# Kernel optimization log

Hardware: AMD Instinct MI355X
Metric: run time of the kernel (lower is better)

The kernel has to match this reference:

```python
import jax, jax.numpy as jnp
import numpy as np

B, T, D = 4, 2048, 2048
NUM_EXPERTS = 64
TOP_K = 2


def setup_inputs() -> dict:
    key = jax.random.key(0)
    k_x, k_n, k_wg, k_wn = jax.random.split(key, 4)
    x = jax.random.normal(k_x, (B, T, D), dtype=jnp.float32)
    noise_eps = jax.random.normal(k_n, (B, T, NUM_EXPERTS), dtype=jnp.float32)
    # nn.Linear(D, E, bias=False): weight [E, D]; store transposed [D, E] for einsum
    scale = 1.0 / np.sqrt(D)
    w_gate = jax.random.uniform(k_wg, (D, NUM_EXPERTS), jnp.float32, -scale, scale)
    w_noise = jax.random.uniform(k_wn, (D, NUM_EXPERTS), jnp.float32, -scale, scale)
    return {"x": x, "noise_eps": noise_eps, "w_gate": w_gate, "w_noise": w_noise}


def reference(x, noise_eps, w_gate, w_noise):
    # gate + noisy logits: softplus(w_noise(x)) * randn_like (noise_eps passed in)
    logits = jnp.einsum("btd,de->bte", x, w_gate)
    noise = jax.nn.softplus(jnp.einsum("btd,de->bte", x, w_noise)) * noise_eps
    logits = logits + noise

    # top-k over experts
    top_k_logits, top_k_indices = jax.lax.top_k(logits, TOP_K)  # [B,T,K]

    # scatter(-inf fill) + softmax == softmax over top-k values scattered into E slots
    one_hot = jax.nn.one_hot(top_k_indices, NUM_EXPERTS, dtype=logits.dtype)  # [B,T,K,E]
    router_probs = jnp.einsum("btk,btke->bte", jax.nn.softmax(top_k_logits, axis=-1), one_hot)

    # per-expert mask: [num_tokens, K, E] -> permute(1,0,2) -> [K, num_tokens, E]
    exp_mask = one_hot.reshape(B * T, TOP_K, NUM_EXPERTS).transpose(1, 0, 2).astype(jnp.int32)
    return router_probs, top_k_indices, exp_mask
```

## Files before the change

kernel.cpp:

```cpp
#include <hip/hip_runtime.h>
#include <math.h>

#define DD     2048
#define EE     64
#define NTOK   8192
#define BM     64
#define KSPLIT 4
#define KQ     512
#define BK     64
#define NCH    (KQ / BK)

#define PROB_OFF 0
#define IDX_OFF  524288
#define MASK_OFF 540672
#define MASK_K_STRIDE (NTOK * EE)

#define XBUF_OFF(b) ((b) * 16384)
#define BBUF_OFF(b) (32768 + (b) * 32768)
#define LDS_BYTES   98304

typedef __bf16 bf16x8 __attribute__((ext_vector_type(8)));
typedef float  f32x16 __attribute__((ext_vector_type(16)));

__device__ __forceinline__ unsigned f2bf_rne(float f) {
  unsigned u = __float_as_uint(f);
  return (u + 0x7fffu + ((u >> 16) & 1u)) >> 16;
}
__device__ __forceinline__ float bf2f(unsigned h) {
  return __uint_as_float(h << 16);
}

__device__ __forceinline__ void gl_lds16(const void* g, void* l) {
  __builtin_amdgcn_global_load_lds(
      (const __attribute__((address_space(1))) unsigned int*)g,
      (__attribute__((address_space(3))) unsigned int*)l,
      16, 0, 0);
}

__global__ __launch_bounds__(256) void prep_w(
    const float* __restrict__ wg, const float* __restrict__ wn,
    unsigned char* __restrict__ wsb)
{
  const int t  = blockIdx.x * 256 + threadIdx.x;
  const int l  = t & 63;
  const int nt = (t >> 6) & 3;
  const int g  = t >> 8;
  const int colg = nt * 32 + (l & 31);
  const int kb   = g * 16 + 8 * (l >> 5);
  const float* wsrc = (colg < EE) ? (wg + colg) : (wn + (colg - EE));

  unsigned hv[8], lv[8];
#pragma unroll
  for (int i = 0; i < 8; ++i) {
    const float v = wsrc[(size_t)(kb + i) * EE];
    const unsigned h = f2bf_rne(v);
    hv[i] = h;
    lv[i] = f2bf_rne(v - bf2f(h));
  }
  uint4 hq, lq;
  hq.x = hv[0] | (hv[1] << 16); hq.y = hv[2] | (hv[3] << 16);
  hq.z = hv[4] | (hv[5] << 16); hq.w = hv[6] | (hv[7] << 16);
  lq.x = lv[0] | (lv[1] << 16); lq.y = lv[2] | (lv[3] << 16);
  lq.z = lv[4] | (lv[5] << 16); lq.w = lv[6] | (lv[7] << 16);

  const size_t base = ((size_t)(g * 4 + nt) * 2) * 1024 + (size_t)l * 16;
  *reinterpret_cast<uint4*>(wsb + base)        = hq;
  *reinterpret_cast<uint4*>(wsb + base + 1024) = lq;
}

union BF8 { bf16x8 v; ushort u[8]; };

__device__ __forceinline__ void cvt_hilo(const float4& a, const float4& b,
                                         bf16x8& hi, bf16x8& lo) {
  const float f[8] = {a.x, a.y, a.z, a.w, b.x, b.y, b.z, b.w};
  BF8 H, L;
#pragma unroll
  for (int i = 0; i < 8; ++i) {
    const unsigned u = __float_as_uint(f[i]);
    H.u[i] = (ushort)(u >> 16);
    L.v[i] = (__bf16)(f[i] - __uint_as_float(u & 0xffff0000u));
  }
  hi = H.v; lo = L.v;
}

__device__ __forceinline__ bf16x8 bc(const uint4& q) {
  return __builtin_bit_cast(bf16x8, q);
}

__global__ __launch_bounds__(512, 2) void router_gemm(
    const float* __restrict__ x,
    const unsigned char* __restrict__ wsb,
    float* __restrict__ part)
{
  __shared__ unsigned char lds[LDS_BYTES];

  const int tid  = threadIdx.x;
  const int wid  = tid >> 6;
  const int lane = tid & 63;
  const int mh   = wid >> 2;
  const int nt   = wid & 3;
  const int tok0 = blockIdx.x * BM;
  const int ks   = blockIdx.y;
  const int kbase = ks * KQ;

  const int xrow  = tid >> 4;
  const int xslot = tid & 15;
  const float* xsrc0 = x + (size_t)(tok0 + xrow) * DD + kbase
                         + ((xslot ^ (xrow & 7)) << 2);
  const float* xsrc1 = x + (size_t)(tok0 + 32 + xrow) * DD + kbase
                         + ((xslot ^ (xrow & 7)) << 2);
  const unsigned char* bsrc = wsb + (size_t)(ks * (KQ / 16)) * 8192
                                  + (size_t)tid * 16;

  const int arow = lane & 31;
  const int atl  = lane >> 5;
  const int xswz = arow & 7;

  f32x16 acc = {0.f,0.f,0.f,0.f,0.f,0.f,0.f,0.f,
                0.f,0.f,0.f,0.f,0.f,0.f,0.f,0.f};

  auto STAGE = [&](int cc, int b) {
    gl_lds16(xsrc0 + cc * BK, &lds[XBUF_OFF(b) + tid * 16]);
    gl_lds16(xsrc1 + cc * BK, &lds[XBUF_OFF(b) + 8192 + tid * 16]);
    const unsigned char* bs = bsrc + (size_t)cc * 32768;
#pragma unroll
    for (int j = 0; j < 4; ++j)
      gl_lds16(bs + j * 8192, &lds[BBUF_OFF(b) + j * 8192 + tid * 16]);
  };

  STAGE(0, 0);
  STAGE(1, 1);

#pragma unroll
  for (int c = 0; c < NCH; ++c) {
    if (c < NCH - 1) asm volatile("s_waitcnt vmcnt(6)" ::: "memory");
    else             asm volatile("s_waitcnt vmcnt(0)" ::: "memory");
    __builtin_amdgcn_s_barrier();
    __builtin_amdgcn_sched_barrier(0);

    const unsigned char* xb = &lds[XBUF_OFF(c & 1)];
    const unsigned char* bb = &lds[BBUF_OFF(c & 1)];
    __builtin_amdgcn_s_setprio(1);
#pragma unroll
    for (int s = 0; s < 4; ++s) {
      const int sl0 = (4 * s + 2 * atl) ^ xswz;
      const int sl1 = (4 * s + 2 * atl + 1) ^ xswz;
      const float4 xa = *reinterpret_cast<const float4*>(
          xb + (32 * mh + arow) * 256 + sl0 * 16);
      const float4 xv = *reinterpret_cast<const float4*>(
          xb + (32 * mh + arow) * 256 + sl1 * 16);
      const unsigned char* q = bb + s * 8192 + nt * 2048 + lane * 16;
      const uint4 bh = *reinterpret_cast<const uint4*>(q);
      const uint4 bl = *reinterpret_cast<const uint4*>(q + 1024);

      bf16x8 ahi, alo;
      cvt_hilo(xa, xv, ahi, alo);
      acc = __builtin_amdgcn_mfma_f32_32x32x16_bf16(ahi, bc(bh), acc, 0, 0, 0);
      acc = __builtin_amdgcn_mfma_f32_32x32x16_bf16(ahi, bc(bl), acc, 0, 0, 0);
      acc = __builtin_amdgcn_mfma_f32_32x32x16_bf16(alo, bc(bh), acc, 0, 0, 0);
    }
    __builtin_amdgcn_s_setprio(0);

    asm volatile("s_waitcnt lgkmcnt(0)" ::: "memory");
    __builtin_amdgcn_s_barrier();
    __builtin_amdgcn_sched_barrier(0);

    if (c + 2 < NCH) STAGE(c + 2, c & 1);
  }

  float* Lp = reinterpret_cast<float*>(lds);
  const int ccol = nt * 32 + (lane & 31);
#pragma unroll
  for (int q = 0; q < 16; ++q) {
    const int r = 32 * mh + (q & 3) + 8 * (q >> 2) + 4 * atl;
    Lp[r * 128 + ccol] = acc[q];
  }
  __syncthreads();
#pragma unroll
  for (int rr = 0; rr < 8; ++rr) {
    const int r = 8 * wid + rr;
    const float2 v = *reinterpret_cast<const float2*>(&Lp[r * 128 + 2 * lane]);
    *reinterpret_cast<float2*>(
        part + ((size_t)(tok0 + r) * KSPLIT + ks) * 128 + 2 * lane) = v;
  }
}

__global__ __launch_bounds__(256) void router_epilogue(
    const float* __restrict__ part,
    const float* __restrict__ noise_eps,
    float* __restrict__ out)
{
  const int t    = blockIdx.x * 4 + (threadIdx.x >> 6);
  const int lane = threadIdx.x & 63;

  const float* p = part + (size_t)t * KSPLIT * 128;
  float g = 0.0f, nraw = 0.0f;
#pragma unroll
  for (int s = 0; s < KSPLIT; ++s) {
    g    += p[s * 128 + lane];
    nraw += p[s * 128 + EE + lane];
  }
  const float ep = noise_eps[(size_t)t * EE + lane];

  const float sp = fmaxf(nraw, 0.0f) + log1pf(expf(-fabsf(nraw)));
  const float z  = fmaf(sp, ep, g);

  float v1 = z; int i1 = lane;
#pragma unroll
  for (int off = 32; off >= 1; off >>= 1) {
    const float ov = __shfl_xor(v1, off, 64);
    const int   oi = __shfl_xor(i1, off, 64);
    if (ov > v1 || (ov == v1 && oi < i1)) { v1 = ov; i1 = oi; }
  }
  float v2 = (lane == i1) ? -INFINITY : z; int i2 = lane;
#pragma unroll
  for (int off = 32; off >= 1; off >>= 1) {
    const float ov = __shfl_xor(v2, off, 64);
    const int   oi = __shfl_xor(i2, off, 64);
    if (ov > v2 || (ov == v2 && oi < i2)) { v2 = ov; i2 = oi; }
  }

  const float e2 = expf(v2 - v1);
  const float denom = 1.0f + e2;
  const float p1 = 1.0f / denom;
  const float p2 = e2 / denom;

  out[PROB_OFF + (size_t)t * EE + lane] =
      (lane == i1) ? p1 : ((lane == i2) ? p2 : 0.0f);

  if (lane == 0) {
    out[IDX_OFF + t * 2 + 0] = (float)i1;
    out[IDX_OFF + t * 2 + 1] = (float)i2;
  }

  out[MASK_OFF + 0 * MASK_K_STRIDE + (size_t)t * EE + lane] = (lane == i1) ? 1.0f : 0.0f;
  out[MASK_OFF + 1 * MASK_K_STRIDE + (size_t)t * EE + lane] = (lane == i2) ? 1.0f : 0.0f;
}

extern "C" void kernel_launch(void* const* d_in, const int* in_sizes, int n_in,
                              void* d_out, int out_size, void* d_ws, size_t ws_size,
                              hipStream_t stream) {
  const float* x   = (const float*)d_in[0];
  const float* eps = (const float*)d_in[1];
  const float* wg  = (const float*)d_in[2];
  const float* wn  = (const float*)d_in[3];

  unsigned char* wsb = (unsigned char*)d_ws;
  float* part = (float*)(wsb + (1 << 20));

  prep_w<<<dim3(128), dim3(256), 0, stream>>>(wg, wn, wsb);
  router_gemm<<<dim3(NTOK / BM, KSPLIT), dim3(512), 0, stream>>>(x, wsb, part);
  router_epilogue<<<dim3(NTOK / 4), dim3(256), 0, stream>>>(part, eps,
                                                            (float*)d_out);
}
```

Before: 127.5 us.

## Enlarge router GEMM tile to 256 tokens with 2x2 per-wave MFMA tiles

Reworks the router GEMM so each block covers 256 tokens with an 8-way K split, and each wave computes a 2x2 grid of 32x32 MFMA tiles, reusing A and B fragments across tiles. Weight tiles are loaded once per 256 tokens, and the grid becomes 1D with the K-split index fastest. The LDS-staged coalesced output write is replaced by direct scattered stores of the accumulators. The trade-off is doubling the partial-sum buffer the epilogue must read, fewer blocks, and uncoalesced stores.

```diff
diff --git a/kernel.cpp b/kernel.cpp
--- a/kernel.cpp
+++ b/kernel.cpp
@@ -4,10 +4,10 @@
 #define DD     2048
 #define EE     64
 #define NTOK   8192
-#define BM     64
-#define KSPLIT 4
-#define KQ     512
-#define BK     64
+#define BM     256
+#define KSPLIT 8
+#define KQ     256
+#define BK     32
 #define NCH    (KQ / BK)
 
 #define PROB_OFF 0
@@ -15,8 +15,8 @@
 #define MASK_OFF 540672
 #define MASK_K_STRIDE (NTOK * EE)
 
-#define XBUF_OFF(b) ((b) * 16384)
-#define BBUF_OFF(b) (32768 + (b) * 32768)
+#define XBUF_OFF(b) ((b) * 49152)
+#define BBUF_OFF(b) ((b) * 49152 + 32768)
 #define LDS_BYTES   98304
 
 typedef __bf16 bf16x8 __attribute__((ext_vector_type(8)));
@@ -97,35 +97,35 @@
   const int tid  = threadIdx.x;
   const int wid  = tid >> 6;
   const int lane = tid & 63;
-  const int mh   = wid >> 2;
-  const int nt   = wid & 3;
-  const int tok0 = blockIdx.x * BM;
-  const int ks   = blockIdx.y;
+  const int mh   = wid >> 1;
+  const int ntp  = wid & 1;
+  const int bid  = blockIdx.x;
+  const int ks   = bid & 7;
+  const int mg   = bid >> 3;
+  const int tok0 = mg * BM;
   const int kbase = ks * KQ;
 
-  const int xrow  = tid >> 4;
-  const int xslot = tid & 15;
-  const float* xsrc0 = x + (size_t)(tok0 + xrow) * DD + kbase
-                         + ((xslot ^ (xrow & 7)) << 2);
-  const float* xsrc1 = x + (size_t)(tok0 + 32 + xrow) * DD + kbase
-                         + ((xslot ^ (xrow & 7)) << 2);
-  const unsigned char* bsrc = wsb + (size_t)(ks * (KQ / 16)) * 8192
-                                  + (size_t)tid * 16;
+  const int xsl = tid & 7;
+  const unsigned char* bsrc = wsb + (size_t)ks * 131072 + (size_t)tid * 16;
 
   const int arow = lane & 31;
   const int atl  = lane >> 5;
   const int xswz = arow & 7;
 
-  f32x16 acc = {0.f,0.f,0.f,0.f,0.f,0.f,0.f,0.f,
-                0.f,0.f,0.f,0.f,0.f,0.f,0.f,0.f};
+  f32x16 a00 = {0.f,0.f,0.f,0.f,0.f,0.f,0.f,0.f,0.f,0.f,0.f,0.f,0.f,0.f,0.f,0.f};
+  f32x16 a01 = a00, a10 = a00, a11 = a00;
 
   auto STAGE = [&](int cc, int b) {
-    gl_lds16(xsrc0 + cc * BK, &lds[XBUF_OFF(b) + tid * 16]);
-    gl_lds16(xsrc1 + cc * BK, &lds[XBUF_OFF(b) + 8192 + tid * 16]);
-    const unsigned char* bs = bsrc + (size_t)cc * 32768;
-#pragma unroll
-    for (int j = 0; j < 4; ++j)
-      gl_lds16(bs + j * 8192, &lds[BBUF_OFF(b) + j * 8192 + tid * 16]);
+#pragma unroll
+    for (int j = 0; j < 4; ++j) {
+      const int row = j * 64 + (tid >> 3);
+      const float* src = x + (size_t)(tok0 + row) * DD + kbase + cc * BK
+                           + ((xsl ^ (row & 7)) << 2);
+      gl_lds16(src, &lds[XBUF_OFF(b) + j * 8192 + tid * 16]);
+    }
+    const unsigned char* bs = bsrc + (size_t)cc * 16384;
+    gl_lds16(bs,        &lds[BBUF_OFF(b) + tid * 16]);
+    gl_lds16(bs + 8192, &lds[BBUF_OFF(b) + 8192 + tid * 16]);
   };
 
   STAGE(0, 0);
@@ -142,22 +142,34 @@
     const unsigned char* bb = &lds[BBUF_OFF(c & 1)];
     __builtin_amdgcn_s_setprio(1);
 #pragma unroll
-    for (int s = 0; s < 4; ++s) {
-      const int sl0 = (4 * s + 2 * atl) ^ xswz;
-      const int sl1 = (4 * s + 2 * atl + 1) ^ xswz;
-      const float4 xa = *reinterpret_cast<const float4*>(
-          xb + (32 * mh + arow) * 256 + sl0 * 16);
-      const float4 xv = *reinterpret_cast<const float4*>(
-          xb + (32 * mh + arow) * 256 + sl1 * 16);
-      const unsigned char* q = bb + s * 8192 + nt * 2048 + lane * 16;
-      const uint4 bh = *reinterpret_cast<const uint4*>(q);
-      const uint4 bl = *reinterpret_cast<const uint4*>(q + 1024);
-
-      bf16x8 ahi, alo;
-      cvt_hilo(xa, xv, ahi, alo);
-      acc = __builtin_amdgcn_mfma_f32_32x32x16_bf16(ahi, bc(bh), acc, 0, 0, 0);
-      acc = __builtin_amdgcn_mfma_f32_32x32x16_bf16(ahi, bc(bl), acc, 0, 0, 0);
-      acc = __builtin_amdgcn_mfma_f32_32x32x16_bf16(alo, bc(bh), acc, 0, 0, 0);
+    for (int s = 0; s < 2; ++s) {
+      bf16x8 ahi[2], alo[2];
+#pragma unroll
+      for (int g = 0; g < 2; ++g) {
+        const int r = 64 * mh + 32 * g + arow;
+        const int sl0 = (4 * s + 2 * atl) ^ xswz;
+        const int sl1 = (4 * s + 2 * atl + 1) ^ xswz;
+        const float4 xa = *reinterpret_cast<const float4*>(
+            xb + r * 128 + sl0 * 16);
+        const float4 xv = *reinterpret_cast<const float4*>(
+            xb + r * 128 + sl1 * 16);
+        cvt_hilo(xa, xv, ahi[g], alo[g]);
+      }
+#pragma unroll
+      for (int t = 0; t < 2; ++t) {
+        const int ntg = 2 * ntp + t;
+        const unsigned char* q = bb + s * 8192 + ntg * 2048 + lane * 16;
+        const uint4 bh = *reinterpret_cast<const uint4*>(q);
+        const uint4 bl = *reinterpret_cast<const uint4*>(q + 1024);
+        f32x16& r0 = t ? a01 : a00;
+        f32x16& r1 = t ? a11 : a10;
+        r0 = __builtin_amdgcn_mfma_f32_32x32x16_bf16(ahi[0], bc(bh), r0, 0, 0, 0);
+        r0 = __builtin_amdgcn_mfma_f32_32x32x16_bf16(ahi[0], bc(bl), r0, 0, 0, 0);
+        r0 = __builtin_amdgcn_mfma_f32_32x32x16_bf16(alo[0], bc(bh), r0, 0, 0, 0);
+        r1 = __builtin_amdgcn_mfma_f32_32x32x16_bf16(ahi[1], bc(bh), r1, 0, 0, 0);
+        r1 = __builtin_amdgcn_mfma_f32_32x32x16_bf16(ahi[1], bc(bl), r1, 0, 0, 0);
+        r1 = __builtin_amdgcn_mfma_f32_32x32x16_bf16(alo[1], bc(bh), r1, 0, 0, 0);
+      }
     }
     __builtin_amdgcn_s_setprio(0);
 
@@ -168,20 +180,19 @@
     if (c + 2 < NCH) STAGE(c + 2, c & 1);
   }
 
-  float* Lp = reinterpret_cast<float*>(lds);
-  const int ccol = nt * 32 + (lane & 31);
-#pragma unroll
-  for (int q = 0; q < 16; ++q) {
-    const int r = 32 * mh + (q & 3) + 8 * (q >> 2) + 4 * atl;
-    Lp[r * 128 + ccol] = acc[q];
-  }
-  __syncthreads();
-#pragma unroll
-  for (int rr = 0; rr < 8; ++rr) {
-    const int r = 8 * wid + rr;
-    const float2 v = *reinterpret_cast<const float2*>(&Lp[r * 128 + 2 * lane]);
-    *reinterpret_cast<float2*>(
-        part + ((size_t)(tok0 + r) * KSPLIT + ks) * 128 + 2 * lane) = v;
+#pragma unroll
+  for (int g = 0; g < 2; ++g) {
+#pragma unroll
+    for (int t = 0; t < 2; ++t) {
+      const f32x16& a = g ? (t ? a11 : a10) : (t ? a01 : a00);
+      const int colb = 64 * ntp + 32 * t + (lane & 31);
+#pragma unroll
+      for (int q = 0; q < 16; ++q) {
+        const int tok = tok0 + 64 * mh + 32 * g
+                      + (q & 3) + 8 * (q >> 2) + 4 * atl;
+        part[((size_t)tok * KSPLIT + ks) * 128 + colb] = a[q];
+      }
+    }
   }
 }
 
@@ -249,7 +260,8 @@
   float* part = (float*)(wsb + (1 << 20));
 
   prep_w<<<dim3(128), dim3(256), 0, stream>>>(wg, wn, wsb);
-  router_gemm<<<dim3(NTOK / BM, KSPLIT), dim3(512), 0, stream>>>(x, wsb, part);
+  router_gemm<<<dim3((NTOK / BM) * KSPLIT), dim3(512), 0, stream>>>(x, wsb,
+                                                                    part);
   router_epilogue<<<dim3(NTOK / 4), dim3(256), 0, stream>>>(part, eps,
                                                             (float*)d_out);
 }
```

Result: faster. 122.7 us (-3.8%).
